# Optimization experiments

Measured on AMD Instinct MI355X. Metric: run time of the kernel, lower is better.

Reference implementation:

```python
import jax, jax.numpy as jnp
import numpy as np

A, U, ANT, D2, H = 128, 8, 64, 64, 256
NUE = A * U            # 1024 ues
E_INT = A * NUE        # 131072 interferes edges (all ap x ue pairs)
E_DL = NUE             # one d_link edge per ue


def _mlp(x, Wa, ba, Wb, bb):
    return jax.nn.relu(x @ Wa + ba) @ Wb + bb


def setup_inputs() -> dict:
    key = jax.random.key(0)
    ks = jax.random.split(key, 14)
    f32 = jnp.float32
    inp = {
        'pl_int_re': jax.random.normal(ks[0], (E_INT, ANT), f32) * 0.1,
        'pl_int_im': jax.random.normal(ks[1], (E_INT, ANT), f32) * 0.1,
        'pl_dl_re': jax.random.normal(ks[2], (E_DL, ANT), f32) * 0.1,
        'pl_dl_im': jax.random.normal(ks[3], (E_DL, ANT), f32) * 0.1,
        'pv_re': jax.random.normal(ks[4], (A, U, ANT), f32) * 0.1,
        'pv_im': jax.random.normal(ks[5], (A, U, ANT), f32) * 0.1,
        'W2a': jax.random.normal(ks[6], (4 * ANT, H), f32) / np.sqrt(4 * ANT),
        'b2a': jnp.zeros((H,), f32),
        'W2b': jax.random.normal(ks[7], (H, D2), f32) / np.sqrt(H),
        'b2b': jnp.zeros((D2,), f32),
        'W1a': jax.random.normal(ks[8], (1 + 2 * ANT + D2, H), f32) / np.sqrt(1 + 2 * ANT + D2),
        'b1a': jnp.zeros((H,), f32),
        'W1b': jax.random.normal(ks[9], (H, 2 * ANT), f32) / np.sqrt(H),
        'b1b': jnp.zeros((2 * ANT,), f32),
        # interferes: every ap -> every ue
        'int_src': jnp.repeat(jnp.arange(A, dtype=jnp.int32), NUE),
        'int_dst': jnp.tile(jnp.arange(NUE, dtype=jnp.int32), A),
        # d_link: ap a -> ues [a*U, (a+1)*U)
        'dl_src': jnp.repeat(jnp.arange(A, dtype=jnp.int32), U),
        'dl_dst': jnp.arange(NUE, dtype=jnp.int32),
    }
    return inp


def reference(pl_int_re, pl_int_im, pl_dl_re, pl_dl_im, pv_re, pv_im,
              W2a, b2a, W2b, b2b, W1a, b1a, W1b, b1b,
              int_src, int_dst, dl_src, dl_dst):
    pv = jax.lax.complex(pv_re, pv_im)            # [A,U,ANT] ap power_vector
    pl_int = jax.lax.complex(pl_int_re, pl_int_im)  # [E_INT,ANT]
    pl_dl = jax.lax.complex(pl_dl_re, pl_dl_im)     # [E_DL,ANT]

    def aggregate_interferes(pv_cur):
        src_sum = jnp.sum(pv_cur, axis=1)[int_src]              # [E,ANT]
        infer_vec = src_sum.conj() * pl_int                      # [E,ANT]
        sum_ap = jnp.sum(jnp.abs(infer_vec) ** 2, axis=-1)       # ||.||^2 -> [E]
        return jax.ops.segment_sum(sum_ap[:, None], int_dst, num_segments=NUE)  # [NUE,1]

    # 1) aggregate_interferes (stored in graph; recomputed at the end)
    _ = aggregate_interferes(pv)

    # 2) mlp_aggregate_interferes
    src_sum = jnp.sum(pv, axis=1)[int_src]                       # [E,ANT] complex
    feats = jnp.concatenate([pl_int, src_sum], axis=1)           # [E,2*ANT] complex
    cat_feats = jnp.concatenate([feats.real, feats.imag], axis=1)  # [E,4*ANT]
    msg2 = _mlp(cat_feats, W2a, b2a, W2b, b2b)                   # [E,D2]
    mlp_ue_all = jax.ops.segment_sum(msg2, int_dst, num_segments=NUE)  # [NUE,D2]

    # 3) update_ue_power_vector (d_link edges)
    src_pv_dl = pv[dl_src]                                       # [E_DL,U,ANT]
    iner = jnp.einsum('eua,ea->eu', src_pv_dl.conj(), pl_dl)     # bmm -> [E_DL,U]
    norm1 = jnp.abs(iner) ** 2                                   # [E_DL,U]
    mask1 = jnp.ones((E_DL, U), norm1.dtype).at[jnp.arange(E_DL), dl_dst % U].set(0.0)
    in_infer = jnp.sum(norm1 * mask1, axis=1)[:, None]           # [E_DL,1]

    feat1 = jnp.concatenate([in_infer, pl_dl.real, pl_dl.imag, mlp_ue_all[dl_dst]], axis=1)
    out1 = _mlp(feat1, W1a, b1a, W1b, b1b).reshape(E_DL, 2, ANT)  # [E_DL,2,ANT]
    ue_pv_msg = jax.lax.complex(out1[:, 0, :], out1[:, 1, :])    # [E_DL,ANT]
    # each ue receives exactly one message
    ue_pv = jnp.zeros((NUE, ANT), ue_pv_msg.dtype).at[dl_dst].set(ue_pv_msg)

    # 4) update_ap_power_vector (u_link: ue i -> ap i//U; mailbox [A,U,ANT])
    mailbox = ue_pv.reshape(A, U, ANT)
    flat = mailbox.reshape(A, U * ANT)
    row_sums = jnp.sum(jnp.abs(flat), axis=-1, keepdims=True)
    pv_new = (flat / row_sums).reshape(A, U, ANT)

    # 5) final aggregate_interferes with updated power vectors
    ue_all_interference = aggregate_interferes(pv_new)

    out_stacked = jnp.stack([pv_new.real, pv_new.imag])          # [2,A,U,ANT]
    return out_stacked, ue_all_interference
```

## Files before the change

kernel.cpp:

```cpp
#include <hip/hip_runtime.h>
#include <hip/hip_bf16.h>
#include <hip/hip_fp16.h>

#define A_NUM 128
#define U_NUM 8
#define ANT 64
#define D2 64
#define H_DIM 256
#define NUE 1024
#define E_INT 131072

typedef __attribute__((ext_vector_type(8))) short bf16x8_t;
typedef __attribute__((ext_vector_type(4))) float f32x4_t;

static __device__ inline unsigned short f2bf(float x) {
    unsigned int u = __float_as_uint(x);
    unsigned int r = (u + 0x7fffu + ((u >> 16) & 1u)) >> 16;
    return (unsigned short)r;
}
static __device__ inline unsigned int pack2(float a, float b) {
    return (unsigned int)f2bf(a) | ((unsigned int)f2bf(b) << 16);
}
static __device__ inline unsigned int packh2(float a, float b) {
    return (unsigned int)__half_as_ushort(__float2half(a)) |
           ((unsigned int)__half_as_ushort(__float2half(b)) << 16);
}

__global__ void prep_kernel(const float* __restrict__ pv_re, const float* __restrict__ pv_im,
                            const float* __restrict__ W2a, const float* __restrict__ b2a,
                            const float* __restrict__ W2b,
                            const float* __restrict__ W1a, const float* __restrict__ W1b,
                            float* __restrict__ Sa, unsigned short* __restrict__ WpF,
                            unsigned short* __restrict__ W2bF,
                            float* __restrict__ W1aT, float* __restrict__ W1bT) {
    int bid = blockIdx.x, t = threadIdx.x;
    if (bid < A_NUM) {
        __shared__ float sre[ANT], sim[ANT];
        if (t < ANT) {
            float s = 0.f;
            for (int u = 0; u < U_NUM; ++u) s += pv_re[bid * 512 + u * 64 + t];
            sre[t] = s;
        } else if (t < 2 * ANT) {
            int ant = t - ANT;
            float s = 0.f;
            for (int u = 0; u < U_NUM; ++u) s += pv_im[bid * 512 + u * 64 + ant];
            sim[ant] = s;
        }
        __syncthreads();
        float a0 = 0.f, a1 = 0.f, a2 = 0.f, a3 = 0.f;
        for (int ant = 0; ant < ANT; ant += 2) {
            a0 += sre[ant] * W2a[(64 + ant) * H_DIM + t];
            a1 += sim[ant] * W2a[(192 + ant) * H_DIM + t];
            a2 += sre[ant + 1] * W2a[(64 + ant + 1) * H_DIM + t];
            a3 += sim[ant + 1] * W2a[(192 + ant + 1) * H_DIM + t];
        }
        Sa[bid * H_DIM + t] = b2a[t] + ((a0 + a2) + (a1 + a3));
    } else if (bid < 136) {
        int base = (bid - A_NUM) * 256 + t;
        for (int f = base; f < 32768 + 16384; f += 8 * 256) {
            if (f < 32768) {
                int i = f & 7, lml = (f >> 3) & 15, lkl = (f >> 7) & 3;
                int kc = (f >> 9) & 3, ht = (f >> 11) & 1, w = (f >> 12) & 3, hh = (f >> 14) & 1;
                int h = hh * 128 + w * 32 + ht * 16 + lml;
                int k = kc * 32 + lkl * 8 + i;
                int row = (k < 64) ? k : (k + 64);
                WpF[f] = f2bf(W2a[row * H_DIM + h]);
            } else {
                int f2 = f - 32768;
                int i = f2 & 7, lml = (f2 >> 3) & 15, lkl = (f2 >> 7) & 3;
                int dt = (f2 >> 9) & 3, w = (f2 >> 11) & 3, hh = (f2 >> 13) & 1;
                int d = dt * 16 + lml;
                int k = hh * 128 + w * 32 + lkl * 8 + i;
                W2bF[f2] = f2bf(W2b[k * D2 + d]);
            }
        }
    } else {
        for (int i = (bid - 136) * 256 + t; i < 53248 + 32768; i += 32 * 256) {
            if (i < 53248) {
                int k = i >> 8, h = i & 255;
                W1aT[h * 208 + k] = (k < 193) ? W1a[k * 256 + h] : 0.f;
            } else {
                int i2 = i - 53248;
                int k = i2 >> 7, c = i2 & 127;
                W1bT[c * 256 + k] = W1b[k * 128 + c];
            }
        }
    }
}

__global__ __launch_bounds__(256) void mlp2_kernel(
        const float* __restrict__ plre, const float* __restrict__ plim,
        const float* __restrict__ Sa, const unsigned short* __restrict__ WpF,
        const unsigned short* __restrict__ W2bF, float* __restrict__ partial,
        unsigned short* __restrict__ Pws) {
    __shared__ __attribute__((aligned(16))) unsigned short Wl[16384];
    __shared__ __attribute__((aligned(16))) unsigned short W2l[8192];
    __shared__ __attribute__((aligned(16))) unsigned short F2[2][4352];
    __shared__ __attribute__((aligned(16))) unsigned short Hw_all[4][1280];
    int bid = blockIdx.x;
    int ac = bid >> 6, hh = (bid >> 5) & 1, jt = bid & 31;
    int j0 = jt * 32, a0 = ac * 8;
    int t = threadIdx.x, w = t >> 6, l = t & 63, lm = l & 15, lk = l >> 4;

    {
        const uint4* srcW = reinterpret_cast<const uint4*>(WpF + hh * 16384);
        const uint4* srcW2 = reinterpret_cast<const uint4*>(W2bF + hh * 8192);
        uint4* dW = reinterpret_cast<uint4*>(Wl);
        uint4* dW2 = reinterpret_cast<uint4*>(W2l);
        for (int q = t; q < 3072; q += 256) {
            if (q < 2048) dW[q] = srcW[q];
            else dW2[q - 2048] = srcW2[q - 2048];
        }
    }

    int er = t >> 3, sg = t & 7;
    const float* sb = (sg < 4) ? plre : plim;
    int soff = (j0 + er) * 64 + (sg & 3) * 16;
    int fw = er * 136 + sg * 16;

    unsigned short* Hw = Hw_all[w];
    f32x4_t acc2[4][2];
#pragma unroll
    for (int dt = 0; dt < 4; ++dt)
#pragma unroll
        for (int jg = 0; jg < 2; ++jg) acc2[dt][jg] = (f32x4_t){0.f, 0.f, 0.f, 0.f};

    float4 s0, s1, s2, s3;
    {
        const float* p = sb + (size_t)a0 * 65536 + soff;
        s0 = *reinterpret_cast<const float4*>(p);
        s1 = *reinterpret_cast<const float4*>(p + 4);
        s2 = *reinterpret_cast<const float4*>(p + 8);
        s3 = *reinterpret_cast<const float4*>(p + 12);
        *reinterpret_cast<uint4*>(&F2[0][fw]) =
            make_uint4(pack2(s0.x, s0.y), pack2(s0.z, s0.w),
                       pack2(s1.x, s1.y), pack2(s1.z, s1.w));
        *reinterpret_cast<uint4*>(&F2[0][fw + 8]) =
            make_uint4(pack2(s2.x, s2.y), pack2(s2.z, s2.w),
                       pack2(s3.x, s3.y), pack2(s3.z, s3.w));
    }
    {
        const float* p = sb + (size_t)(a0 + 1) * 65536 + soff;
        s0 = *reinterpret_cast<const float4*>(p);
        s1 = *reinterpret_cast<const float4*>(p + 4);
        s2 = *reinterpret_cast<const float4*>(p + 8);
        s3 = *reinterpret_cast<const float4*>(p + 12);
    }
    __syncthreads();

    int cur = 0;
    for (int ai = 0; ai < 8; ++ai) {
        int a = a0 + ai;
        const unsigned short* Fc = F2[cur];

        if (hh == 0) {
            uint4 rr = *reinterpret_cast<const uint4*>(Fc + er * 136 + sg * 8);
            uint4 ri = *reinterpret_cast<const uint4*>(Fc + er * 136 + 64 + sg * 8);
            const unsigned short* pr = (const unsigned short*)&rr;
            const unsigned short* pi = (const unsigned short*)&ri;
            unsigned int pk[4];
#pragma unroll
            for (int i = 0; i < 4; ++i) {
                float re0 = __uint_as_float(((unsigned int)pr[2 * i]) << 16);
                float im0 = __uint_as_float(((unsigned int)pi[2 * i]) << 16);
                float re1 = __uint_as_float(((unsigned int)pr[2 * i + 1]) << 16);
                float im1 = __uint_as_float(((unsigned int)pi[2 * i + 1]) << 16);
                pk[i] = packh2(re0 * re0 + im0 * im0, re1 * re1 + im1 * im1);
            }
            *reinterpret_cast<uint4*>(&Pws[(unsigned)(a * 1024 + j0 + er) * 64 + sg * 8]) =
                make_uint4(pk[0], pk[1], pk[2], pk[3]);
        }

        float sa0 = Sa[a * H_DIM + hh * 128 + w * 32 + lm];
        float sa1 = Sa[a * H_DIM + hh * 128 + w * 32 + 16 + lm];
        f32x4_t acc1[2][2];
        acc1[0][0] = (f32x4_t){sa0, sa0, sa0, sa0};
        acc1[1][0] = acc1[0][0];
        acc1[0][1] = (f32x4_t){sa1, sa1, sa1, sa1};
        acc1[1][1] = acc1[0][1];
#pragma unroll
        for (int kc = 0; kc < 4; ++kc) {
            bf16x8_t b0 = *reinterpret_cast<const bf16x8_t*>(Wl + ((w * 2 + 0) * 4 + kc) * 512 + l * 8);
            bf16x8_t b1 = *reinterpret_cast<const bf16x8_t*>(Wl + ((w * 2 + 1) * 4 + kc) * 512 + l * 8);
            bf16x8_t aA = *reinterpret_cast<const bf16x8_t*>(Fc + lm * 136 + kc * 32 + lk * 8);
            bf16x8_t aB = *reinterpret_cast<const bf16x8_t*>(Fc + (16 + lm) * 136 + kc * 32 + lk * 8);
            acc1[0][0] = __builtin_amdgcn_mfma_f32_16x16x32_bf16(aA, b0, acc1[0][0], 0, 0, 0);
            acc1[0][1] = __builtin_amdgcn_mfma_f32_16x16x32_bf16(aA, b1, acc1[0][1], 0, 0, 0);
            acc1[1][0] = __builtin_amdgcn_mfma_f32_16x16x32_bf16(aB, b0, acc1[1][0], 0, 0, 0);
            acc1[1][1] = __builtin_amdgcn_mfma_f32_16x16x32_bf16(aB, b1, acc1[1][1], 0, 0, 0);
        }
#pragma unroll
        for (int jg = 0; jg < 2; ++jg)
#pragma unroll
            for (int ht = 0; ht < 2; ++ht)
#pragma unroll
                for (int r = 0; r < 4; ++r) {
                    float v = acc1[jg][ht][r];
                    Hw[(jg * 16 + lk * 4 + r) * 40 + ht * 16 + lm] = f2bf(v > 0.f ? v : 0.f);
                }
        {
            bf16x8_t a20 = *reinterpret_cast<const bf16x8_t*>(Hw + lm * 40 + lk * 8);
            bf16x8_t a21 = *reinterpret_cast<const bf16x8_t*>(Hw + (16 + lm) * 40 + lk * 8);
#pragma unroll
            for (int dt = 0; dt < 4; ++dt) {
                bf16x8_t b2 = *reinterpret_cast<const bf16x8_t*>(W2l + (w * 4 + dt) * 512 + l * 8);
                acc2[dt][0] = __builtin_amdgcn_mfma_f32_16x16x32_bf16(a20, b2, acc2[dt][0], 0, 0, 0);
                acc2[dt][1] = __builtin_amdgcn_mfma_f32_16x16x32_bf16(a21, b2, acc2[dt][1], 0, 0, 0);
            }
        }
        if (ai < 7) {
            *reinterpret_cast<uint4*>(&F2[cur ^ 1][fw]) =
                make_uint4(pack2(s0.x, s0.y), pack2(s0.z, s0.w),
                           pack2(s1.x, s1.y), pack2(s1.z, s1.w));
            *reinterpret_cast<uint4*>(&F2[cur ^ 1][fw + 8]) =
                make_uint4(pack2(s2.x, s2.y), pack2(s2.z, s2.w),
                           pack2(s3.x, s3.y), pack2(s3.z, s3.w));
            if (ai < 6) {
                const float* p = sb + (size_t)(a0 + ai + 2) * 65536 + soff;
                s0 = *reinterpret_cast<const float4*>(p);
                s1 = *reinterpret_cast<const float4*>(p + 4);
                s2 = *reinterpret_cast<const float4*>(p + 8);
                s3 = *reinterpret_cast<const float4*>(p + 12);
            }
            __syncthreads();
            cur ^= 1;
        }
    }

    __syncthreads();
    float* red = reinterpret_cast<float*>(Wl);
#pragma unroll
    for (int dt = 0; dt < 4; ++dt)
#pragma unroll
        for (int jg = 0; jg < 2; ++jg)
#pragma unroll
            for (int r = 0; r < 4; ++r)
                red[(w * 32 + jg * 16 + lk * 4 + r) * 64 + dt * 16 + lm] = acc2[dt][jg][r];
    __syncthreads();
    for (int idx = t; idx < 2048; idx += 256) {
        int j = idx >> 6, d = idx & 63;
        float s = (red[(0 * 32 + j) * 64 + d] + red[(1 * 32 + j) * 64 + d]) +
                  (red[(2 * 32 + j) * 64 + d] + red[(3 * 32 + j) * 64 + d]);
        partial[(hh * 16 + ac) * 65536 + (j0 + j) * 64 + d] = s;
    }
}

__global__ __launch_bounds__(512) void dlink_norm(
        const float* __restrict__ pv_re, const float* __restrict__ pv_im,
        const float* __restrict__ pldre, const float* __restrict__ pldim,
        const float* __restrict__ partial, const float* __restrict__ b2b,
        const float* __restrict__ W1aT, const float* __restrict__ b1a,
        const float* __restrict__ W1bT, const float* __restrict__ b1b,
        float* __restrict__ Q, float* __restrict__ out) {
    int a = blockIdx.x, t = threadIdx.x, w = t >> 6, l = t & 63;
    __shared__ float pvr[512], pvi[512], pldr[512], pldi[512];
    __shared__ float nrm[8][8];
    __shared__ __attribute__((aligned(16))) float feat[8][212];
    __shared__ __attribute__((aligned(16))) float h1[8][260];
    __shared__ float red2[2][8][128];
    __shared__ __attribute__((aligned(16))) float o1[8][128];
    __shared__ float redn[8];
    __shared__ float SshInv;

    pvr[t] = pv_re[a * 512 + t];
    pvi[t] = pv_im[a * 512 + t];
    pldr[t] = pldre[a * 512 + t];
    pldi[t] = pldim[a * 512 + t];
    {
        float acc = 128.f * b2b[t & 63];
#pragma unroll
        for (int c = 0; c < 32; ++c) acc += partial[c * 65536 + a * 512 + t];
        feat[t >> 6][129 + (t & 63)] = acc;
    }
    if (t < 152) feat[t / 19][193 + t % 19] = 0.f;
    __syncthreads();
    feat[t >> 6][1 + (t & 63)] = pldr[t];
    feat[t >> 6][65 + (t & 63)] = pldi[t];
#pragma unroll
    for (int p = 0; p < 8; ++p) {
        int idx = w * 8 + p;
        int el = idx >> 3, u = idx & 7;
        float pr = pvr[u * 64 + l], pi = pvi[u * 64 + l];
        float qr = pldr[el * 64 + l], qi = pldi[el * 64 + l];
        float ir = pr * qr + pi * qi;
        float ii = pr * qi - pi * qr;
        for (int m = 1; m < 64; m <<= 1) {
            ir += __shfl_xor(ir, m, 64);
            ii += __shfl_xor(ii, m, 64);
        }
        if (l == 0) nrm[el][u] = ir * ir + ii * ii;
    }
    __syncthreads();
    if (t < 8) {
        float s = 0.f;
        for (int u = 0; u < 8; ++u)
            if (u != t) s += nrm[t][u];
        feat[t][0] = s;
    }
    __syncthreads();
    {
        int h = t >> 1, e0 = (t & 1) * 4;
        const float4* wrow = reinterpret_cast<const float4*>(W1aT + h * 208);
        const float4* f0p = reinterpret_cast<const float4*>(&feat[e0 + 0][0]);
        const float4* f1p = reinterpret_cast<const float4*>(&feat[e0 + 1][0]);
        const float4* f2p = reinterpret_cast<const float4*>(&feat[e0 + 2][0]);
        const float4* f3p = reinterpret_cast<const float4*>(&feat[e0 + 3][0]);
        float ac0 = 0.f, ac1 = 0.f, ac2 = 0.f, ac3 = 0.f;
#pragma unroll 4
        for (int kq = 0; kq < 52; ++kq) {
            float4 wv = wrow[kq];
            float4 f0 = f0p[kq], f1 = f1p[kq], f2 = f2p[kq], f3 = f3p[kq];
            ac0 = fmaf(wv.x, f0.x, ac0); ac0 = fmaf(wv.y, f0.y, ac0);
            ac0 = fmaf(wv.z, f0.z, ac0); ac0 = fmaf(wv.w, f0.w, ac0);
            ac1 = fmaf(wv.x, f1.x, ac1); ac1 = fmaf(wv.y, f1.y, ac1);
            ac1 = fmaf(wv.z, f1.z, ac1); ac1 = fmaf(wv.w, f1.w, ac1);
            ac2 = fmaf(wv.x, f2.x, ac2); ac2 = fmaf(wv.y, f2.y, ac2);
            ac2 = fmaf(wv.z, f2.z, ac2); ac2 = fmaf(wv.w, f2.w, ac2);
            ac3 = fmaf(wv.x, f3.x, ac3); ac3 = fmaf(wv.y, f3.y, ac3);
            ac3 = fmaf(wv.z, f3.z, ac3); ac3 = fmaf(wv.w, f3.w, ac3);
        }
        float bb = b1a[h];
        float s0 = bb + ac0, s1 = bb + ac1, s2 = bb + ac2, s3 = bb + ac3;
        h1[e0 + 0][h] = s0 > 0.f ? s0 : 0.f;
        h1[e0 + 1][h] = s1 > 0.f ? s1 : 0.f;
        h1[e0 + 2][h] = s2 > 0.f ? s2 : 0.f;
        h1[e0 + 3][h] = s3 > 0.f ? s3 : 0.f;
    }
    __syncthreads();
    {
        int e0 = (t & 1) * 4, c = (t >> 1) & 127, kh = t >> 8;
        const float4* wrow = reinterpret_cast<const float4*>(W1bT + c * 256 + kh * 128);
        const float4* g0 = reinterpret_cast<const float4*>(&h1[e0 + 0][kh * 128]);
        const float4* g1 = reinterpret_cast<const float4*>(&h1[e0 + 1][kh * 128]);
        const float4* g2 = reinterpret_cast<const float4*>(&h1[e0 + 2][kh * 128]);
        const float4* g3 = reinterpret_cast<const float4*>(&h1[e0 + 3][kh * 128]);
        float ac0 = 0.f, ac1 = 0.f, ac2 = 0.f, ac3 = 0.f;
#pragma unroll 4
        for (int kq = 0; kq < 32; ++kq) {
            float4 wv = wrow[kq];
            float4 f0 = g0[kq], f1 = g1[kq], f2 = g2[kq], f3 = g3[kq];
            ac0 = fmaf(wv.x, f0.x, ac0); ac0 = fmaf(wv.y, f0.y, ac0);
            ac0 = fmaf(wv.z, f0.z, ac0); ac0 = fmaf(wv.w, f0.w, ac0);
            ac1 = fmaf(wv.x, f1.x, ac1); ac1 = fmaf(wv.y, f1.y, ac1);
            ac1 = fmaf(wv.z, f1.z, ac1); ac1 = fmaf(wv.w, f1.w, ac1);
            ac2 = fmaf(wv.x, f2.x, ac2); ac2 = fmaf(wv.y, f2.y, ac2);
            ac2 = fmaf(wv.z, f2.z, ac2); ac2 = fmaf(wv.w, f2.w, ac2);
            ac3 = fmaf(wv.x, f3.x, ac3); ac3 = fmaf(wv.y, f3.y, ac3);
            ac3 = fmaf(wv.z, f3.z, ac3); ac3 = fmaf(wv.w, f3.w, ac3);
        }
        red2[kh][e0 + 0][c] = ac0;
        red2[kh][e0 + 1][c] = ac1;
        red2[kh][e0 + 2][c] = ac2;
        red2[kh][e0 + 3][c] = ac3;
    }
    __syncthreads();
    {
        int i0 = t, i1 = t + 512;
        o1[i0 >> 7][i0 & 127] = b1b[i0 & 127] + red2[0][i0 >> 7][i0 & 127] + red2[1][i0 >> 7][i0 & 127];
        o1[i1 >> 7][i1 & 127] = b1b[i1 & 127] + red2[0][i1 >> 7][i1 & 127] + red2[1][i1 >> 7][i1 & 127];
    }
    __syncthreads();
    {
        int el = t >> 6, ant = t & 63;
        float re = o1[el][ant], im = o1[el][64 + ant];
        float v = sqrtf(re * re + im * im);
        for (int m = 1; m < 64; m <<= 1) v += __shfl_xor(v, m, 64);
        if (l == 0) redn[w] = v;
    }
    __syncthreads();
    if (t == 0) {
        float S = redn[0] + redn[1] + redn[2] + redn[3] +
                  redn[4] + redn[5] + redn[6] + redn[7];
        SshInv = 1.f / S;
    }
    __syncthreads();
    {
        float inv = SshInv;
        int el = t >> 6, ant = t & 63;
        out[a * 512 + t] = o1[el][ant] * inv;
        out[65536 + a * 512 + t] = o1[el][64 + ant] * inv;
        if (t < 64) {
            float sr = 0.f, si = 0.f;
#pragma unroll
            for (int u = 0; u < 8; ++u) {
                sr += o1[u][t];
                si += o1[u][64 + t];
            }
            sr *= inv;
            si *= inv;
            Q[a * 64 + t] = sr * sr + si * si;
        }
    }
}

__global__ __launch_bounds__(256) void final_agg(const unsigned short* __restrict__ Pws,
                                                 const float* __restrict__ Qv,
                                                 float* __restrict__ out) {
    int bid = blockIdx.x, t = threadIdx.x, w = t >> 6, l = t & 63;
    __shared__ __attribute__((aligned(16))) float Qc[128][68];
    for (int i = t; i < 8192; i += 256) Qc[i >> 6][i & 63] = Qv[i];
    __syncthreads();
    int j = bid * 4 + w;
    int as = l >> 3, og = l & 7;
    float acc = 0.f;
#pragma unroll 4
    for (int ab = 0; ab < 16; ++ab) {
        int aa = ab * 8 + as;
        uint4 pv4 = *reinterpret_cast<const uint4*>(&Pws[(unsigned)(aa * 1024 + j) * 64 + og * 8]);
        float4 q0 = *reinterpret_cast<const float4*>(&Qc[aa][og * 8]);
        float4 q1 = *reinterpret_cast<const float4*>(&Qc[aa][og * 8 + 4]);
        const unsigned short* hp = (const unsigned short*)&pv4;
        acc += __half2float(__ushort_as_half(hp[0])) * q0.x;
        acc += __half2float(__ushort_as_half(hp[1])) * q0.y;
        acc += __half2float(__ushort_as_half(hp[2])) * q0.z;
        acc += __half2float(__ushort_as_half(hp[3])) * q0.w;
        acc += __half2float(__ushort_as_half(hp[4])) * q1.x;
        acc += __half2float(__ushort_as_half(hp[5])) * q1.y;
        acc += __half2float(__ushort_as_half(hp[6])) * q1.z;
        acc += __half2float(__ushort_as_half(hp[7])) * q1.w;
    }
    for (int m = 1; m < 64; m <<= 1) acc += __shfl_xor(acc, m, 64);
    if (l == 0) out[131072 + j] = acc;
}

extern "C" void kernel_launch(void* const* d_in, const int* in_sizes, int n_in,
                              void* d_out, int out_size, void* d_ws, size_t ws_size,
                              hipStream_t stream) {
    const float* plre = (const float*)d_in[0];
    const float* plim = (const float*)d_in[1];
    const float* pldre = (const float*)d_in[2];
    const float* pldim = (const float*)d_in[3];
    const float* pvre = (const float*)d_in[4];
    const float* pvim = (const float*)d_in[5];
    const float* W2a = (const float*)d_in[6];
    const float* b2a = (const float*)d_in[7];
    const float* W2b = (const float*)d_in[8];
    const float* b2b = (const float*)d_in[9];
    const float* W1a = (const float*)d_in[10];
    const float* b1a = (const float*)d_in[11];
    const float* W1b = (const float*)d_in[12];
    const float* b1b = (const float*)d_in[13];

    char* ws = (char*)d_ws;
    float* Sa = (float*)(ws);
    unsigned short* WpF = (unsigned short*)(ws + 131072);
    unsigned short* W2bF = (unsigned short*)(ws + 196608);
    float* Q = (float*)(ws + 229376);
    float* W1aT = (float*)(ws + 262144);
    float* W1bT = (float*)(ws + 475136);
    float* partial = (float*)(ws + 606208);
    unsigned short* Pws = (unsigned short*)(ws + 8994816);
    float* out = (float*)d_out;

    prep_kernel<<<168, 256, 0, stream>>>(pvre, pvim, W2a, b2a, W2b, W1a, W1b,
                                         Sa, WpF, W2bF, W1aT, W1bT);
    mlp2_kernel<<<1024, 256, 0, stream>>>(plre, plim, Sa, WpF, W2bF, partial, Pws);
    dlink_norm<<<128, 512, 0, stream>>>(pvre, pvim, pldre, pldim, partial, b2b,
                                        W1aT, b1a, W1bT, b1b, Q, out);
    final_agg<<<256, 256, 0, stream>>>(Pws, Q, out);
}
```

Baseline: 76.42 us.

## Restructure MLP2 kernel: 512-thread blocks, register-resident hidden layer, transposed MFMA

The mlp2 kernel now uses 512 threads per block with 64-edge tiles, splitting waves across edge halves and hidden-column quarters. The first-layer MFMA is transposed (weights as A operand), so its output fragment can be ReLU'd, converted to bf16 in registers, and fed directly into a 16x16x16 MFMA for the second layer. This removes the per-wave LDS round-trip for the hidden activations and the W2 fragment layout is reshaped to match. The feature double buffer is replaced by a single buffer with an extra barrier, and the cross-wave reduction becomes a staged pairwise add through LDS. The extra barriers and the smaller grid may reduce overlap.

```diff
diff --git a/kernel.cpp b/kernel.cpp
--- a/kernel.cpp
+++ b/kernel.cpp
@@ -11,6 +11,7 @@
 #define E_INT 131072
 
 typedef __attribute__((ext_vector_type(8))) short bf16x8_t;
+typedef __attribute__((ext_vector_type(4))) short bf16x4_t;
 typedef __attribute__((ext_vector_type(4))) float f32x4_t;
 
 static __device__ inline unsigned short f2bf(float x) {
@@ -24,6 +25,16 @@
 static __device__ inline unsigned int packh2(float a, float b) {
     return (unsigned int)__half_as_ushort(__float2half(a)) |
            ((unsigned int)__half_as_ushort(__float2half(b)) << 16);
+}
+static __device__ inline bf16x4_t relu_cvt4(f32x4_t v) {
+    float t0 = v[0] > 0.f ? v[0] : 0.f;
+    float t1 = v[1] > 0.f ? v[1] : 0.f;
+    float t2 = v[2] > 0.f ? v[2] : 0.f;
+    float t3 = v[3] > 0.f ? v[3] : 0.f;
+    union { unsigned int u[2]; bf16x4_t s; } r;
+    r.u[0] = pack2(t0, t1);
+    r.u[1] = pack2(t2, t3);
+    return r.s;
 }
 
 __global__ void prep_kernel(const float* __restrict__ pv_re, const float* __restrict__ pv_im,
@@ -31,7 +42,7 @@
                             const float* __restrict__ W2b,
                             const float* __restrict__ W1a, const float* __restrict__ W1b,
                             float* __restrict__ Sa, unsigned short* __restrict__ WpF,
-                            unsigned short* __restrict__ W2bF,
+                            unsigned short* __restrict__ W2F,
                             float* __restrict__ W1aT, float* __restrict__ W1bT) {
     int bid = blockIdx.x, t = threadIdx.x;
     if (bid < A_NUM) {
@@ -60,18 +71,18 @@
         for (int f = base; f < 32768 + 16384; f += 8 * 256) {
             if (f < 32768) {
                 int i = f & 7, lml = (f >> 3) & 15, lkl = (f >> 7) & 3;
-                int kc = (f >> 9) & 3, ht = (f >> 11) & 1, w = (f >> 12) & 3, hh = (f >> 14) & 1;
-                int h = hh * 128 + w * 32 + ht * 16 + lml;
+                int kc = (f >> 9) & 3, ht8 = (f >> 11) & 7, hh = (f >> 14) & 1;
+                int h = hh * 128 + ht8 * 16 + lml;
                 int k = kc * 32 + lkl * 8 + i;
                 int row = (k < 64) ? k : (k + 64);
                 WpF[f] = f2bf(W2a[row * H_DIM + h]);
             } else {
                 int f2 = f - 32768;
-                int i = f2 & 7, lml = (f2 >> 3) & 15, lkl = (f2 >> 7) & 3;
-                int dt = (f2 >> 9) & 3, w = (f2 >> 11) & 3, hh = (f2 >> 13) & 1;
-                int d = dt * 16 + lml;
-                int k = hh * 128 + w * 32 + lkl * 8 + i;
-                W2bF[f2] = f2bf(W2b[k * D2 + d]);
+                int i = f2 & 3, ll = (f2 >> 2) & 63;
+                int dt = (f2 >> 8) & 3, ht8 = (f2 >> 10) & 7, hh = (f2 >> 13) & 1;
+                int d = dt * 16 + (ll & 15);
+                int k = hh * 128 + ht8 * 16 + (ll >> 4) * 4 + i;
+                W2F[f2] = f2bf(W2b[k * D2 + d]);
             }
         }
     } else {
@@ -88,42 +99,41 @@
     }
 }
 
-__global__ __launch_bounds__(256) void mlp2_kernel(
+__global__ __launch_bounds__(512) void mlp2_kernel(
         const float* __restrict__ plre, const float* __restrict__ plim,
         const float* __restrict__ Sa, const unsigned short* __restrict__ WpF,
-        const unsigned short* __restrict__ W2bF, float* __restrict__ partial,
+        const unsigned short* __restrict__ W2F, float* __restrict__ partial,
         unsigned short* __restrict__ Pws) {
     __shared__ __attribute__((aligned(16))) unsigned short Wl[16384];
     __shared__ __attribute__((aligned(16))) unsigned short W2l[8192];
-    __shared__ __attribute__((aligned(16))) unsigned short F2[2][4352];
-    __shared__ __attribute__((aligned(16))) unsigned short Hw_all[4][1280];
+    __shared__ __attribute__((aligned(16))) unsigned short Fbuf[8704];
     int bid = blockIdx.x;
-    int ac = bid >> 6, hh = (bid >> 5) & 1, jt = bid & 31;
-    int j0 = jt * 32, a0 = ac * 8;
-    int t = threadIdx.x, w = t >> 6, l = t & 63, lm = l & 15, lk = l >> 4;
-
-    {
-        const uint4* srcW = reinterpret_cast<const uint4*>(WpF + hh * 16384);
-        const uint4* srcW2 = reinterpret_cast<const uint4*>(W2bF + hh * 8192);
+    int ac = bid >> 5, hh = (bid >> 4) & 1, jtile = bid & 15;
+    int j0 = jtile * 64, a0 = ac * 8;
+    int t = threadIdx.x, l = t & 63, lm = l & 15, lk = l >> 4;
+    int wv = t >> 6, jw = wv >> 2, hw = wv & 3;
+
+    {
+        const uint4* sW = reinterpret_cast<const uint4*>(WpF + hh * 16384);
+        const uint4* sW2 = reinterpret_cast<const uint4*>(W2F + hh * 8192);
         uint4* dW = reinterpret_cast<uint4*>(Wl);
         uint4* dW2 = reinterpret_cast<uint4*>(W2l);
-        for (int q = t; q < 3072; q += 256) {
-            if (q < 2048) dW[q] = srcW[q];
-            else dW2[q - 2048] = srcW2[q - 2048];
+        for (int q = t; q < 3072; q += 512) {
+            if (q < 2048) dW[q] = sW[q];
+            else dW2[q - 2048] = sW2[q - 2048];
         }
     }
 
     int er = t >> 3, sg = t & 7;
     const float* sb = (sg < 4) ? plre : plim;
     int soff = (j0 + er) * 64 + (sg & 3) * 16;
-    int fw = er * 136 + sg * 16;
-
-    unsigned short* Hw = Hw_all[w];
+    int fw = er * 136 + ((sg < 4) ? 0 : 64) + (sg & 3) * 16;
+
     f32x4_t acc2[4][2];
 #pragma unroll
     for (int dt = 0; dt < 4; ++dt)
 #pragma unroll
-        for (int jg = 0; jg < 2; ++jg) acc2[dt][jg] = (f32x4_t){0.f, 0.f, 0.f, 0.f};
+        for (int jt = 0; jt < 2; ++jt) acc2[dt][jt] = (f32x4_t){0.f, 0.f, 0.f, 0.f};
 
     float4 s0, s1, s2, s3;
     {
@@ -132,10 +142,10 @@
         s1 = *reinterpret_cast<const float4*>(p + 4);
         s2 = *reinterpret_cast<const float4*>(p + 8);
         s3 = *reinterpret_cast<const float4*>(p + 12);
-        *reinterpret_cast<uint4*>(&F2[0][fw]) =
+        *reinterpret_cast<uint4*>(&Fbuf[fw]) =
             make_uint4(pack2(s0.x, s0.y), pack2(s0.z, s0.w),
                        pack2(s1.x, s1.y), pack2(s1.z, s1.w));
-        *reinterpret_cast<uint4*>(&F2[0][fw + 8]) =
+        *reinterpret_cast<uint4*>(&Fbuf[fw + 8]) =
             make_uint4(pack2(s2.x, s2.y), pack2(s2.z, s2.w),
                        pack2(s3.x, s3.y), pack2(s3.z, s3.w));
     }
@@ -148,14 +158,11 @@
     }
     __syncthreads();
 
-    int cur = 0;
     for (int ai = 0; ai < 8; ++ai) {
         int a = a0 + ai;
-        const unsigned short* Fc = F2[cur];
-
         if (hh == 0) {
-            uint4 rr = *reinterpret_cast<const uint4*>(Fc + er * 136 + sg * 8);
-            uint4 ri = *reinterpret_cast<const uint4*>(Fc + er * 136 + 64 + sg * 8);
+            uint4 rr = *reinterpret_cast<const uint4*>(Fbuf + er * 136 + sg * 8);
+            uint4 ri = *reinterpret_cast<const uint4*>(Fbuf + er * 136 + 64 + sg * 8);
             const unsigned short* pr = (const unsigned short*)&rr;
             const unsigned short* pi = (const unsigned short*)&ri;
             unsigned int pk[4];
@@ -170,49 +177,47 @@
             *reinterpret_cast<uint4*>(&Pws[(unsigned)(a * 1024 + j0 + er) * 64 + sg * 8]) =
                 make_uint4(pk[0], pk[1], pk[2], pk[3]);
         }
-
-        float sa0 = Sa[a * H_DIM + hh * 128 + w * 32 + lm];
-        float sa1 = Sa[a * H_DIM + hh * 128 + w * 32 + 16 + lm];
         f32x4_t acc1[2][2];
-        acc1[0][0] = (f32x4_t){sa0, sa0, sa0, sa0};
-        acc1[1][0] = acc1[0][0];
-        acc1[0][1] = (f32x4_t){sa1, sa1, sa1, sa1};
-        acc1[1][1] = acc1[0][1];
+#pragma unroll
+        for (int ht = 0; ht < 2; ++ht) {
+            f32x4_t sa = *reinterpret_cast<const f32x4_t*>(
+                Sa + a * H_DIM + hh * 128 + hw * 32 + ht * 16 + lk * 4);
+            acc1[ht][0] = sa;
+            acc1[ht][1] = sa;
+        }
 #pragma unroll
         for (int kc = 0; kc < 4; ++kc) {
-            bf16x8_t b0 = *reinterpret_cast<const bf16x8_t*>(Wl + ((w * 2 + 0) * 4 + kc) * 512 + l * 8);
-            bf16x8_t b1 = *reinterpret_cast<const bf16x8_t*>(Wl + ((w * 2 + 1) * 4 + kc) * 512 + l * 8);
-            bf16x8_t aA = *reinterpret_cast<const bf16x8_t*>(Fc + lm * 136 + kc * 32 + lk * 8);
-            bf16x8_t aB = *reinterpret_cast<const bf16x8_t*>(Fc + (16 + lm) * 136 + kc * 32 + lk * 8);
-            acc1[0][0] = __builtin_amdgcn_mfma_f32_16x16x32_bf16(aA, b0, acc1[0][0], 0, 0, 0);
-            acc1[0][1] = __builtin_amdgcn_mfma_f32_16x16x32_bf16(aA, b1, acc1[0][1], 0, 0, 0);
-            acc1[1][0] = __builtin_amdgcn_mfma_f32_16x16x32_bf16(aB, b0, acc1[1][0], 0, 0, 0);
-            acc1[1][1] = __builtin_amdgcn_mfma_f32_16x16x32_bf16(aB, b1, acc1[1][1], 0, 0, 0);
-        }
-#pragma unroll
-        for (int jg = 0; jg < 2; ++jg)
-#pragma unroll
-            for (int ht = 0; ht < 2; ++ht)
-#pragma unroll
-                for (int r = 0; r < 4; ++r) {
-                    float v = acc1[jg][ht][r];
-                    Hw[(jg * 16 + lk * 4 + r) * 40 + ht * 16 + lm] = f2bf(v > 0.f ? v : 0.f);
-                }
-        {
-            bf16x8_t a20 = *reinterpret_cast<const bf16x8_t*>(Hw + lm * 40 + lk * 8);
-            bf16x8_t a21 = *reinterpret_cast<const bf16x8_t*>(Hw + (16 + lm) * 40 + lk * 8);
+            bf16x8_t aw0 = *reinterpret_cast<const bf16x8_t*>(
+                Wl + (((hw * 2 + 0) * 4 + kc) << 9) + l * 8);
+            bf16x8_t aw1 = *reinterpret_cast<const bf16x8_t*>(
+                Wl + (((hw * 2 + 1) * 4 + kc) << 9) + l * 8);
+            bf16x8_t bf0 = *reinterpret_cast<const bf16x8_t*>(
+                Fbuf + (jw * 32 + lm) * 136 + kc * 32 + lk * 8);
+            bf16x8_t bf1 = *reinterpret_cast<const bf16x8_t*>(
+                Fbuf + (jw * 32 + 16 + lm) * 136 + kc * 32 + lk * 8);
+            acc1[0][0] = __builtin_amdgcn_mfma_f32_16x16x32_bf16(aw0, bf0, acc1[0][0], 0, 0, 0);
+            acc1[0][1] = __builtin_amdgcn_mfma_f32_16x16x32_bf16(aw0, bf1, acc1[0][1], 0, 0, 0);
+            acc1[1][0] = __builtin_amdgcn_mfma_f32_16x16x32_bf16(aw1, bf0, acc1[1][0], 0, 0, 0);
+            acc1[1][1] = __builtin_amdgcn_mfma_f32_16x16x32_bf16(aw1, bf1, acc1[1][1], 0, 0, 0);
+        }
+#pragma unroll
+        for (int ht = 0; ht < 2; ++ht) {
+            bf16x4_t hl0 = relu_cvt4(acc1[ht][0]);
+            bf16x4_t hl1 = relu_cvt4(acc1[ht][1]);
 #pragma unroll
             for (int dt = 0; dt < 4; ++dt) {
-                bf16x8_t b2 = *reinterpret_cast<const bf16x8_t*>(W2l + (w * 4 + dt) * 512 + l * 8);
-                acc2[dt][0] = __builtin_amdgcn_mfma_f32_16x16x32_bf16(a20, b2, acc2[dt][0], 0, 0, 0);
-                acc2[dt][1] = __builtin_amdgcn_mfma_f32_16x16x32_bf16(a21, b2, acc2[dt][1], 0, 0, 0);
+                bf16x4_t w2 = *reinterpret_cast<const bf16x4_t*>(
+                    W2l + (((hw * 2 + ht) * 4 + dt) << 8) + l * 4);
+                acc2[dt][0] = __builtin_amdgcn_mfma_f32_16x16x16bf16_1k(w2, hl0, acc2[dt][0], 0, 0, 0);
+                acc2[dt][1] = __builtin_amdgcn_mfma_f32_16x16x16bf16_1k(w2, hl1, acc2[dt][1], 0, 0, 0);
             }
         }
         if (ai < 7) {
-            *reinterpret_cast<uint4*>(&F2[cur ^ 1][fw]) =
+            __syncthreads();
+            *reinterpret_cast<uint4*>(&Fbuf[fw]) =
                 make_uint4(pack2(s0.x, s0.y), pack2(s0.z, s0.w),
                            pack2(s1.x, s1.y), pack2(s1.z, s1.w));
-            *reinterpret_cast<uint4*>(&F2[cur ^ 1][fw + 8]) =
+            *reinterpret_cast<uint4*>(&Fbuf[fw + 8]) =
                 make_uint4(pack2(s2.x, s2.y), pack2(s2.z, s2.w),
                            pack2(s3.x, s3.y), pack2(s3.z, s3.w));
             if (ai < 6) {
@@ -223,26 +228,49 @@
                 s3 = *reinterpret_cast<const float4*>(p + 12);
             }
             __syncthreads();
-            cur ^= 1;
-        }
-    }
-
-    __syncthreads();
-    float* red = reinterpret_cast<float*>(Wl);
-#pragma unroll
-    for (int dt = 0; dt < 4; ++dt)
-#pragma unroll
-        for (int jg = 0; jg < 2; ++jg)
-#pragma unroll
-            for (int r = 0; r < 4; ++r)
-                red[(w * 32 + jg * 16 + lk * 4 + r) * 64 + dt * 16 + lm] = acc2[dt][jg][r];
-    __syncthreads();
-    for (int idx = t; idx < 2048; idx += 256) {
-        int j = idx >> 6, d = idx & 63;
-        float s = (red[(0 * 32 + j) * 64 + d] + red[(1 * 32 + j) * 64 + d]) +
-                  (red[(2 * 32 + j) * 64 + d] + red[(3 * 32 + j) * 64 + d]);
-        partial[(hh * 16 + ac) * 65536 + (j0 + j) * 64 + d] = s;
-    }
+        }
+    }
+
+    float* R = reinterpret_cast<float*>(Fbuf);
+#define STORE_R()                                                              \
+    do {                                                                       \
+        _Pragma("unroll") for (int dt = 0; dt < 4; ++dt)                       \
+            _Pragma("unroll") for (int jt = 0; jt < 2; ++jt)                   \
+                *reinterpret_cast<f32x4_t*>(                                   \
+                    &R[(jw * 32 + jt * 16 + lm) * 68 + dt * 16 + lk * 4]) =    \
+                    acc2[dt][jt];                                              \
+    } while (0)
+#define ADD_R()                                                                \
+    do {                                                                       \
+        _Pragma("unroll") for (int dt = 0; dt < 4; ++dt)                       \
+            _Pragma("unroll") for (int jt = 0; jt < 2; ++jt)                   \
+                acc2[dt][jt] += *reinterpret_cast<const f32x4_t*>(             \
+                    &R[(jw * 32 + jt * 16 + lm) * 68 + dt * 16 + lk * 4]);     \
+    } while (0)
+    __syncthreads();
+    if (hw == 1) STORE_R();
+    __syncthreads();
+    if (hw == 0) ADD_R();
+    __syncthreads();
+    if (hw == 3) STORE_R();
+    __syncthreads();
+    if (hw == 2) ADD_R();
+    __syncthreads();
+    if (hw == 2) STORE_R();
+    __syncthreads();
+    if (hw == 0) {
+        ADD_R();
+#pragma unroll
+        for (int dt = 0; dt < 4; ++dt)
+#pragma unroll
+            for (int jt = 0; jt < 2; ++jt)
+                *reinterpret_cast<float4*>(
+                    &partial[(size_t)(hh * 16 + ac) * 65536 +
+                             (j0 + jw * 32 + jt * 16 + lm) * 64 + dt * 16 + lk * 4]) =
+                    *reinterpret_cast<float4*>(&acc2[dt][jt]);
+    }
+#undef STORE_R
+#undef ADD_R
 }
 
 __global__ __launch_bounds__(512) void dlink_norm(
@@ -317,7 +345,7 @@
             ac2 = fmaf(wv.x, f2.x, ac2); ac2 = fmaf(wv.y, f2.y, ac2);
             ac2 = fmaf(wv.z, f2.z, ac2); ac2 = fmaf(wv.w, f2.w, ac2);
             ac3 = fmaf(wv.x, f3.x, ac3); ac3 = fmaf(wv.y, f3.y, ac3);
-            ac3 = fmaf(wv.z, f3.z, ac3); ac3 = fmaf(wv.w, f3.w, ac3);
+            ac3 = fmaf(wv.w, f3.w, ac3); ac3 = fmaf(wv.z, f3.z, ac3);
         }
         float bb = b1a[h];
         float s0 = bb + ac0, s1 = bb + ac1, s2 = bb + ac2, s3 = bb + ac3;
@@ -444,7 +472,7 @@
     char* ws = (char*)d_ws;
     float* Sa = (float*)(ws);
     unsigned short* WpF = (unsigned short*)(ws + 131072);
-    unsigned short* W2bF = (unsigned short*)(ws + 196608);
+    unsigned short* W2F = (unsigned short*)(ws + 196608);
     float* Q = (float*)(ws + 229376);
     float* W1aT = (float*)(ws + 262144);
     float* W1bT = (float*)(ws + 475136);
@@ -453,8 +481,8 @@
     float* out = (float*)d_out;
 
     prep_kernel<<<168, 256, 0, stream>>>(pvre, pvim, W2a, b2a, W2b, W1a, W1b,
-                                         Sa, WpF, W2bF, W1aT, W1bT);
-    mlp2_kernel<<<1024, 256, 0, stream>>>(plre, plim, Sa, WpF, W2bF, partial, Pws);
+                                         Sa, WpF, W2F, W1aT, W1bT);
+    mlp2_kernel<<<512, 512, 0, stream>>>(plre, plim, Sa, WpF, W2F, partial, Pws);
     dlink_norm<<<128, 512, 0, stream>>>(pvre, pvim, pldre, pldim, partial, b2b,
                                         W1aT, b1a, W1bT, b1b, Q, out);
     final_agg<<<256, 256, 0, stream>>>(Pws, Q, out);
```

New measurement: 66.22 us. 1.15x faster.
